# Kernel optimization log

Measured on AMD Instinct MI355X. Metric: run time of the kernel, lower is better.

## Reference

```python
import jax, jax.numpy as jnp
import numpy as np

DIM = 512

def setup_inputs() -> dict:
    key = jax.random.key(0)
    ks = jax.random.split(key, 8)
    B, T, S, D = 4, 128, 512, DIM
    scale = 1.0 / np.sqrt(D)
    return {
        "inp": jax.random.normal(ks[0], (B, T, D), jnp.float32),
        "context": jax.random.normal(ks[1], (B, S, D), jnp.float32),
        # linear_query: Linear(D, D, bias=True)
        "Wq": jax.random.normal(ks[2], (D, D), jnp.float32) * scale,
        "bq": jax.random.normal(ks[3], (D,), jnp.float32) * scale,
        # linear_context: Linear(D, D, bias=False)
        "Wc": jax.random.normal(ks[4], (D, D), jnp.float32) * scale,
        # v: Linear(D, 1, bias=False)
        "v": jax.random.normal(ks[5], (D,), jnp.float32) * scale,
        # linear_out: Linear(2D, D, bias=True)
        "Wout": jax.random.normal(ks[6], (D, 2 * D), jnp.float32) * scale,
        "bout": jax.random.normal(ks[7], (D,), jnp.float32) * scale,
    }

def reference(inp, context, Wq, bq, Wc, v, Wout, bout):
    # inp: (B,T,D) target queries; context: (B,S,D) source states
    wq = jnp.einsum('btd,ed->bte', inp, Wq) + bq          # (B,T,D)
    uh = jnp.einsum('bsd,ed->bse', context, Wc)            # (B,S,D)
    # additive (Bahdanau) score: v^T tanh(Wq q_t + Wc h_s)
    wquh = jnp.tanh(wq[:, :, None, :] + uh[:, None, :, :])  # (B,T,S,D)
    align = jnp.einsum('btsd,d->bts', wquh, v)             # (B,T,S)
    align_vectors = jax.nn.softmax(align, axis=-1)          # softmax over src_len
    c = jnp.einsum('bts,bsd->btd', align_vectors, context)  # context vector
    concat_c = jnp.concatenate([c, inp], axis=-1)           # (B,T,2D)
    attn_h = jnp.einsum('btf,ef->bte', concat_c, Wout) + bout  # (B,T,D)
    return attn_h, align_vectors
```

## Files before the change

### kernel.cpp

```cpp
#include <hip/hip_runtime.h>
#include <hip/hip_bf16.h>
#include <math.h>


typedef __attribute__((ext_vector_type(8))) short short8;
typedef __attribute__((ext_vector_type(4))) float f32x4;
typedef unsigned short ushort_t;

static __device__ __forceinline__ unsigned short f2bf(float x) {
    union { __hip_bfloat16 h; unsigned short u; } c;
    c.h = __float2bfloat16(x);
    return c.u;
}
static __device__ __forceinline__ int bf2x(float lo, float hi) {
    return (int)(((unsigned)f2bf(hi) << 16) | (unsigned)f2bf(lo));
}

template<bool BF>
static __device__ __forceinline__ void load16(const void* base, size_t elemoff,
                                              int4& r0, int4& r1) {
    if (BF) {
        const int4* p = (const int4*)((const ushort_t*)base + elemoff);
        r0 = p[0]; r1 = p[1];
    } else {
        const float4* p = (const float4*)((const float*)base + elemoff);
        float4 a = p[0], b = p[1], c = p[2], d = p[3];
        r0.x = bf2x(a.x, a.y); r0.y = bf2x(a.z, a.w);
        r0.z = bf2x(b.x, b.y); r0.w = bf2x(b.z, b.w);
        r1.x = bf2x(c.x, c.y); r1.y = bf2x(c.z, c.w);
        r1.z = bf2x(d.x, d.y); r1.w = bf2x(d.z, d.w);
    }
}

template<bool A_BF, bool W_BF, int EPI>
static __device__ __forceinline__ void gemm_body(
    ushort_t* As, ushort_t* Ws,
    const void* A, const void* W, const float* bias, const float* partial,
    void* Cv, int K, int lda, int ldw, int ldc, int bm, int bn)
{
    const int tid = threadIdx.x;
    const int wave = tid >> 6, lane = tid & 63;
    const int mh = (wave & 1) * 32, nh = (wave >> 1) * 32;
    const int quad = lane >> 4, l16 = lane & 15;
    const int srow = tid >> 2, schunk = tid & 3;

    const size_t aoff = (size_t)(bm + srow) * lda + schunk * 16;
    const size_t woff = (size_t)(bn + srow) * ldw + schunk * 16;
    int4* AsW = (int4*)&As[srow * 72 + schunk * 16];
    int4* WsW = (int4*)&Ws[srow * 72 + schunk * 16];

    f32x4 acc00 = {0.f, 0.f, 0.f, 0.f}, acc01 = acc00, acc10 = acc00, acc11 = acc00;

    int4 a0r, a1r, w0r, w1r;
    load16<A_BF>(A, aoff, a0r, a1r);
    load16<W_BF>(W, woff, w0r, w1r);

    for (int k0 = 0; k0 < K; k0 += 64) {
        AsW[0] = a0r; AsW[1] = a1r;
        WsW[0] = w0r; WsW[1] = w1r;
        __syncthreads();
        if (k0 + 64 < K) {
            load16<A_BF>(A, aoff + k0 + 64, a0r, a1r);
            load16<W_BF>(W, woff + k0 + 64, w0r, w1r);
        }
        #pragma unroll
        for (int kk = 0; kk < 64; kk += 32) {
            short8 a0 = *(const short8*)&As[(mh + l16) * 72 + kk + quad * 8];
            short8 a1 = *(const short8*)&As[(mh + 16 + l16) * 72 + kk + quad * 8];
            short8 b0 = *(const short8*)&Ws[(nh + l16) * 72 + kk + quad * 8];
            short8 b1 = *(const short8*)&Ws[(nh + 16 + l16) * 72 + kk + quad * 8];
            acc00 = __builtin_amdgcn_mfma_f32_16x16x32_bf16(a0, b0, acc00, 0, 0, 0);
            acc01 = __builtin_amdgcn_mfma_f32_16x16x32_bf16(a0, b1, acc01, 0, 0, 0);
            acc10 = __builtin_amdgcn_mfma_f32_16x16x32_bf16(a1, b0, acc10, 0, 0, 0);
            acc11 = __builtin_amdgcn_mfma_f32_16x16x32_bf16(a1, b1, acc11, 0, 0, 0);
        }
        __syncthreads();
    }

    const int col0 = bn + nh + l16;
    const int col1 = col0 + 16;
    float bias0 = bias ? bias[col0] : 0.f;
    float bias1 = bias ? bias[col1] : 0.f;

    f32x4 accs[2][2] = {{acc00, acc01}, {acc10, acc11}};
    #pragma unroll
    for (int mt = 0; mt < 2; ++mt) {
        #pragma unroll
        for (int r = 0; r < 4; ++r) {
            int row = bm + mh + mt * 16 + quad * 4 + r;
            size_t rowoff = (size_t)row * ldc;
            float v0 = accs[mt][0][r] + bias0;
            float v1 = accs[mt][1][r] + bias1;
            if (EPI == 1) { v0 = __expf(2.f * v0); v1 = __expf(2.f * v1); }
            if (EPI == 3) { v0 += partial[rowoff + col0]; v1 += partial[rowoff + col1]; }
            if (EPI == 2) {
                ushort_t* C = (ushort_t*)Cv;
                C[rowoff + col0] = f2bf(v0);
                C[rowoff + col1] = f2bf(v1);
            } else {
                float* C = (float*)Cv;
                C[rowoff + col0] = v0;
                C[rowoff + col1] = v1;
            }
        }
    }
}

__global__ __launch_bounds__(256) void fused_front(
    const float* __restrict__ inp, const float* __restrict__ ctx,
    const float* __restrict__ Wq, const float* __restrict__ bq,
    const float* __restrict__ Wc, const float* __restrict__ Wout,
    const float* __restrict__ bout,
    float* __restrict__ Ew, float* __restrict__ Eu, float* __restrict__ Y0,
    ushort_t* __restrict__ ctxT)
{
    __shared__ ushort_t As[64 * 72];
    __shared__ ushort_t Ws[64 * 72];
    __shared__ float tile[32][33];
    const int bid = blockIdx.x, tid = threadIdx.x;

    if (bid < 64) {
        gemm_body<false, false, 1>(As, Ws, inp, Wq, bq, nullptr, Ew,
                                   512, 512, 512, 512, (bid & 7) * 64, (bid >> 3) * 64);
    } else if (bid < 320) {
        int i = bid - 64;
        gemm_body<false, false, 1>(As, Ws, ctx, Wc, nullptr, nullptr, Eu,
                                   512, 512, 512, 512, (i & 31) * 64, (i >> 5) * 64);
    } else if (bid < 384) {
        int i = bid - 320;
        gemm_body<false, false, 0>(As, Ws, inp, Wout + 512, bout, nullptr, Y0,
                                   512, 512, 1024, 512, (i & 7) * 64, (i >> 3) * 64);
    } else {
        int r = bid - 384;
        int b = r >> 8;
        int tr = (r >> 4) & 15, tc = r & 15;
        const float* src = ctx + ((size_t)(b * 512 + tr * 32)) * 512 + tc * 32;
        int row8 = tid >> 5, col = tid & 31;
        #pragma unroll
        for (int p = 0; p < 4; ++p) {
            int rr = p * 8 + row8;
            tile[rr][col] = src[rr * 512 + col];
        }
        __syncthreads();
        ushort_t* dst = ctxT + ((size_t)(b * 512 + tc * 32)) * 512 + tr * 32;
        #pragma unroll
        for (int p = 0; p < 4; ++p) {
            int rr = p * 8 + row8;
            dst[rr * 512 + col] = f2bf(tile[col][rr]);
        }
    }
}

__global__ __launch_bounds__(256) void align_kernel(
    const float* __restrict__ Ew, const float* __restrict__ Eu,
    const float* __restrict__ v, float* __restrict__ out)
{
    const int lane = threadIdx.x & 63, wave = threadIdx.x >> 6;
    const int b = blockIdx.z;
    const int t0 = blockIdx.y * 8 + wave * 2;
    const int s0 = blockIdx.x * 8;

    const float* w0p = Ew + (((size_t)(b * 128 + t0)) << 9);
    const float* w1p = w0p + 512;
    const float* up  = Eu + (((size_t)(b * 512 + s0)) << 9);

    float acc0[8], acc1[8];
    #pragma unroll
    for (int j = 0; j < 8; ++j) { acc0[j] = 0.f; acc1[j] = 0.f; }
    float vsum = 0.f;

    for (int k0 = 0; k0 < 512; k0 += 64) {
        float vk = v[k0 + lane];
        vsum += vk;
        float w0 = w0p[k0 + lane];
        float w1 = w1p[k0 + lane];
        #pragma unroll
        for (int j = 0; j < 8; ++j) {
            float u = up[((size_t)j << 9) + k0 + lane];
            float d0 = fmaf(w0, u, 1.f);
            float d1 = fmaf(w1, u, 1.f);
            float r0 = __builtin_amdgcn_rcpf(d0);
            float r1 = __builtin_amdgcn_rcpf(d1);
            acc0[j] = fmaf(vk, r0, acc0[j]);
            acc1[j] = fmaf(vk, r1, acc1[j]);
        }
    }

    float V = vsum;
    #pragma unroll
    for (int off = 32; off; off >>= 1) V += __shfl_xor(V, off, 64);

    float r0 = 0.f, r1 = 0.f;
    #pragma unroll
    for (int j = 0; j < 8; ++j) {
        float a = acc0[j], c = acc1[j];
        #pragma unroll
        for (int off = 32; off; off >>= 1) {
            a += __shfl_xor(a, off, 64);
            c += __shfl_xor(c, off, 64);
        }
        if (lane == j) { r0 = fmaf(-2.f, a, V); r1 = fmaf(-2.f, c, V); }
    }
    if (lane < 8) {
        size_t o = (((size_t)(b * 128 + t0)) << 9) + s0 + lane;
        out[o] = r0;
        out[o + 512] = r1;
    }
}

__global__ __launch_bounds__(256) void softmax_512(
    float* __restrict__ data, ushort_t* __restrict__ pbf)
{
    const int row = blockIdx.x;
    float* p = data + ((size_t)row << 9);
    ushort_t* q = pbf + ((size_t)row << 9);
    const int tid = threadIdx.x;
    float x0 = p[tid];
    float x1 = p[tid + 256];

    float m = fmaxf(x0, x1);
    #pragma unroll
    for (int off = 32; off > 0; off >>= 1)
        m = fmaxf(m, __shfl_xor(m, off, 64));
    __shared__ float redm[4];
    __shared__ float reds[4];
    const int wave = tid >> 6;
    if ((tid & 63) == 0) redm[wave] = m;
    __syncthreads();
    m = fmaxf(fmaxf(redm[0], redm[1]), fmaxf(redm[2], redm[3]));

    float e0 = __expf(x0 - m);
    float e1 = __expf(x1 - m);
    float s = e0 + e1;
    #pragma unroll
    for (int off = 32; off > 0; off >>= 1)
        s += __shfl_xor(s, off, 64);
    if ((tid & 63) == 0) reds[wave] = s;
    __syncthreads();
    s = reds[0] + reds[1] + reds[2] + reds[3];
    float r = 1.0f / s;
    float p0 = e0 * r, p1 = e1 * r;
    p[tid] = p0;
    p[tid + 256] = p1;
    q[tid] = f2bf(p0);
    q[tid + 256] = f2bf(p1);
}

__global__ __launch_bounds__(256) void gemm_c(
    const ushort_t* __restrict__ P, const ushort_t* __restrict__ ctxT,
    ushort_t* __restrict__ cbf)
{
    __shared__ ushort_t As[64 * 72];
    __shared__ ushort_t Ws[64 * 72];
    const int b = blockIdx.z;
    gemm_body<true, true, 2>(As, Ws, P + (size_t)b * 65536, ctxT + (size_t)b * 262144,
                             nullptr, nullptr, cbf + (size_t)b * 65536,
                             512, 512, 512, 512, blockIdx.x * 64, blockIdx.y * 64);
}

__global__ __launch_bounds__(256) void gemm_out(
    const ushort_t* __restrict__ cbf, const float* __restrict__ Wout,
    const float* __restrict__ Y0, float* __restrict__ attn)
{
    __shared__ ushort_t As[64 * 72];
    __shared__ ushort_t Ws[64 * 72];
    gemm_body<true, false, 3>(As, Ws, cbf, Wout, nullptr, Y0, attn,
                              512, 512, 1024, 512, blockIdx.x * 64, blockIdx.y * 64);
}

extern "C" void kernel_launch(void* const* d_in, const int* in_sizes, int n_in,
                              void* d_out, int out_size, void* d_ws, size_t ws_size,
                              hipStream_t stream)
{
    const float* inp  = (const float*)d_in[0];
    const float* ctx  = (const float*)d_in[1];
    const float* Wq   = (const float*)d_in[2];
    const float* bq   = (const float*)d_in[3];
    const float* Wc   = (const float*)d_in[4];
    const float* v    = (const float*)d_in[5];
    const float* Wout = (const float*)d_in[6];
    const float* bout = (const float*)d_in[7];

    float* out   = (float*)d_out;
    float* attn  = out;
    float* align = out + 262144;

    float* ws = (float*)d_ws;
    float* Ew = ws;
    float* Eu = ws + 262144;
    float* Y0 = ws + 1310720;
    ushort_t* ub   = (ushort_t*)(ws + 1572864);
    ushort_t* ctxT = ub;
    ushort_t* P_bf = ub + 1048576;
    ushort_t* c_bf = P_bf + 262144;

    fused_front<<<dim3(1408), 256, 0, stream>>>(inp, ctx, Wq, bq, Wc, Wout, bout,
                                                Ew, Eu, Y0, ctxT);
    align_kernel<<<dim3(64, 16, 4), 256, 0, stream>>>(Ew, Eu, v, align);
    softmax_512<<<dim3(512), 256, 0, stream>>>(align, P_bf);
    gemm_c<<<dim3(2, 8, 4), 256, 0, stream>>>(P_bf, ctxT, c_bf);
    gemm_out<<<dim3(8, 8), 256, 0, stream>>>(c_bf, Wout, Y0, attn);
}
```

Before: 124.5 us.

## Reassociate context-output GEMM and fuse softmax into the attention GEMM

Precomputes G = Wout_c · context^T per batch in the front kernel, replacing the ctx transpose blocks. Attention output then becomes P · G plus Y0 in a single GEMM. Softmax is computed inside that GEMM's prologue, which writes align_vectors and converts P to bf16 on the fly. This removes the separate softmax and two-stage c/out GEMMs, cutting two launches and intermediate traffic. In exchange the front kernel does an extra 512x512x512 GEMM per batch, and the softmax row statistics are recomputed redundantly by every column-tile block.

```diff
diff --git a/kernel.cpp b/kernel.cpp
--- a/kernel.cpp
+++ b/kernel.cpp
@@ -35,7 +35,7 @@
 template<bool A_BF, bool W_BF, int EPI>
 static __device__ __forceinline__ void gemm_body(
     ushort_t* As, ushort_t* Ws,
-    const void* A, const void* W, const float* bias, const float* partial,
+    const void* A, const void* W, const float* bias,
     void* Cv, int K, int lda, int ldw, int ldc, int bm, int bn)
 {
     const int tid = threadIdx.x;
@@ -92,7 +92,6 @@
             float v0 = accs[mt][0][r] + bias0;
             float v1 = accs[mt][1][r] + bias1;
             if (EPI == 1) { v0 = __expf(2.f * v0); v1 = __expf(2.f * v1); }
-            if (EPI == 3) { v0 += partial[rowoff + col0]; v1 += partial[rowoff + col1]; }
             if (EPI == 2) {
                 ushort_t* C = (ushort_t*)Cv;
                 C[rowoff + col0] = f2bf(v0);
@@ -112,42 +111,29 @@
     const float* __restrict__ Wc, const float* __restrict__ Wout,
     const float* __restrict__ bout,
     float* __restrict__ Ew, float* __restrict__ Eu, float* __restrict__ Y0,
-    ushort_t* __restrict__ ctxT)
+    ushort_t* __restrict__ GT)
 {
     __shared__ ushort_t As[64 * 72];
     __shared__ ushort_t Ws[64 * 72];
-    __shared__ float tile[32][33];
-    const int bid = blockIdx.x, tid = threadIdx.x;
+    const int bid = blockIdx.x;
 
     if (bid < 64) {
-        gemm_body<false, false, 1>(As, Ws, inp, Wq, bq, nullptr, Ew,
+        gemm_body<false, false, 1>(As, Ws, inp, Wq, bq, Ew,
                                    512, 512, 512, 512, (bid & 7) * 64, (bid >> 3) * 64);
     } else if (bid < 320) {
         int i = bid - 64;
-        gemm_body<false, false, 1>(As, Ws, ctx, Wc, nullptr, nullptr, Eu,
+        gemm_body<false, false, 1>(As, Ws, ctx, Wc, nullptr, Eu,
                                    512, 512, 512, 512, (i & 31) * 64, (i >> 5) * 64);
-    } else if (bid < 384) {
+    } else if (bid < 576) {
         int i = bid - 320;
-        gemm_body<false, false, 0>(As, Ws, inp, Wout + 512, bout, nullptr, Y0,
+        int b = i >> 6, j = i & 63;
+        gemm_body<false, false, 2>(As, Ws, Wout, ctx + (size_t)b * 262144, nullptr,
+                                   GT + (size_t)b * 262144,
+                                   512, 1024, 512, 512, (j & 7) * 64, (j >> 3) * 64);
+    } else {
+        int i = bid - 576;
+        gemm_body<false, false, 0>(As, Ws, inp, Wout + 512, bout, Y0,
                                    512, 512, 1024, 512, (i & 7) * 64, (i >> 3) * 64);
-    } else {
-        int r = bid - 384;
-        int b = r >> 8;
-        int tr = (r >> 4) & 15, tc = r & 15;
-        const float* src = ctx + ((size_t)(b * 512 + tr * 32)) * 512 + tc * 32;
-        int row8 = tid >> 5, col = tid & 31;
-        #pragma unroll
-        for (int p = 0; p < 4; ++p) {
-            int rr = p * 8 + row8;
-            tile[rr][col] = src[rr * 512 + col];
-        }
-        __syncthreads();
-        ushort_t* dst = ctxT + ((size_t)(b * 512 + tc * 32)) * 512 + tr * 32;
-        #pragma unroll
-        for (int p = 0; p < 4; ++p) {
-            int rr = p * 8 + row8;
-            dst[rr * 512 + col] = f2bf(tile[col][rr]);
-        }
     }
 }
 
@@ -208,64 +194,105 @@
     }
 }
 
-__global__ __launch_bounds__(256) void softmax_512(
-    float* __restrict__ data, ushort_t* __restrict__ pbf)
-{
-    const int row = blockIdx.x;
-    float* p = data + ((size_t)row << 9);
-    ushort_t* q = pbf + ((size_t)row << 9);
-    const int tid = threadIdx.x;
-    float x0 = p[tid];
-    float x1 = p[tid + 256];
-
-    float m = fmaxf(x0, x1);
-    #pragma unroll
-    for (int off = 32; off > 0; off >>= 1)
-        m = fmaxf(m, __shfl_xor(m, off, 64));
-    __shared__ float redm[4];
-    __shared__ float reds[4];
-    const int wave = tid >> 6;
-    if ((tid & 63) == 0) redm[wave] = m;
-    __syncthreads();
-    m = fmaxf(fmaxf(redm[0], redm[1]), fmaxf(redm[2], redm[3]));
-
-    float e0 = __expf(x0 - m);
-    float e1 = __expf(x1 - m);
-    float s = e0 + e1;
-    #pragma unroll
-    for (int off = 32; off > 0; off >>= 1)
-        s += __shfl_xor(s, off, 64);
-    if ((tid & 63) == 0) reds[wave] = s;
-    __syncthreads();
-    s = reds[0] + reds[1] + reds[2] + reds[3];
-    float r = 1.0f / s;
-    float p0 = e0 * r, p1 = e1 * r;
-    p[tid] = p0;
-    p[tid + 256] = p1;
-    q[tid] = f2bf(p0);
-    q[tid + 256] = f2bf(p1);
-}
-
-__global__ __launch_bounds__(256) void gemm_c(
-    const ushort_t* __restrict__ P, const ushort_t* __restrict__ ctxT,
-    ushort_t* __restrict__ cbf)
+__global__ __launch_bounds__(256) void gemm_att(
+    const float* __restrict__ Sraw, const ushort_t* __restrict__ GT,
+    const float* __restrict__ Y0, float* __restrict__ attn,
+    float* __restrict__ alignv)
 {
     __shared__ ushort_t As[64 * 72];
     __shared__ ushort_t Ws[64 * 72];
+    const int tid = threadIdx.x;
     const int b = blockIdx.z;
-    gemm_body<true, true, 2>(As, Ws, P + (size_t)b * 65536, ctxT + (size_t)b * 262144,
-                             nullptr, nullptr, cbf + (size_t)b * 65536,
-                             512, 512, 512, 512, blockIdx.x * 64, blockIdx.y * 64);
-}
-
-__global__ __launch_bounds__(256) void gemm_out(
-    const ushort_t* __restrict__ cbf, const float* __restrict__ Wout,
-    const float* __restrict__ Y0, float* __restrict__ attn)
-{
-    __shared__ ushort_t As[64 * 72];
-    __shared__ ushort_t Ws[64 * 72];
-    gemm_body<true, false, 3>(As, Ws, cbf, Wout, nullptr, Y0, attn,
-                              512, 512, 1024, 512, blockIdx.x * 64, blockIdx.y * 64);
+    const int bm = blockIdx.x * 64;
+    const int bn = blockIdx.y * 64;
+    const int wave = tid >> 6, lane = tid & 63;
+    const int mh = (wave & 1) * 32, nh = (wave >> 1) * 32;
+    const int quad = lane >> 4, l16 = lane & 15;
+    const int srow = tid >> 2, schunk = tid & 3;
+
+    const float* Srow = Sraw + (((size_t)(b * 128 + bm + srow)) << 9);
+
+    const float4* qv = (const float4*)(Srow + schunk * 128);
+    float mloc = -3.4e38f;
+    #pragma unroll
+    for (int i = 0; i < 32; ++i) {
+        float4 x = qv[i];
+        mloc = fmaxf(mloc, fmaxf(fmaxf(x.x, x.y), fmaxf(x.z, x.w)));
+    }
+    mloc = fmaxf(mloc, __shfl_xor(mloc, 1, 64));
+    mloc = fmaxf(mloc, __shfl_xor(mloc, 2, 64));
+    float ssum = 0.f;
+    #pragma unroll
+    for (int i = 0; i < 32; ++i) {
+        float4 x = qv[i];
+        ssum += __expf(x.x - mloc) + __expf(x.y - mloc)
+              + __expf(x.z - mloc) + __expf(x.w - mloc);
+    }
+    ssum += __shfl_xor(ssum, 1, 64);
+    ssum += __shfl_xor(ssum, 2, 64);
+    const float rinv = __builtin_amdgcn_rcpf(ssum);
+
+    const bool wr = (blockIdx.y == 0);
+    float* arow = alignv + (((size_t)(b * 128 + bm + srow)) << 9);
+    const ushort_t* GTb = GT + (size_t)b * 262144;
+    const size_t woff = (size_t)(bn + srow) * 512 + schunk * 16;
+    int4* AsW = (int4*)&As[srow * 72 + schunk * 16];
+    int4* WsW = (int4*)&Ws[srow * 72 + schunk * 16];
+
+    f32x4 acc00 = {0.f, 0.f, 0.f, 0.f}, acc01 = acc00, acc10 = acc00, acc11 = acc00;
+
+    for (int k0 = 0; k0 < 512; k0 += 64) {
+        const float4* ap = (const float4*)(Srow + k0 + schunk * 16);
+        float4 x0 = ap[0], x1 = ap[1], x2 = ap[2], x3 = ap[3];
+        float4 p0, p1, p2, p3;
+        p0.x = __expf(x0.x - mloc) * rinv; p0.y = __expf(x0.y - mloc) * rinv;
+        p0.z = __expf(x0.z - mloc) * rinv; p0.w = __expf(x0.w - mloc) * rinv;
+        p1.x = __expf(x1.x - mloc) * rinv; p1.y = __expf(x1.y - mloc) * rinv;
+        p1.z = __expf(x1.z - mloc) * rinv; p1.w = __expf(x1.w - mloc) * rinv;
+        p2.x = __expf(x2.x - mloc) * rinv; p2.y = __expf(x2.y - mloc) * rinv;
+        p2.z = __expf(x2.z - mloc) * rinv; p2.w = __expf(x2.w - mloc) * rinv;
+        p3.x = __expf(x3.x - mloc) * rinv; p3.y = __expf(x3.y - mloc) * rinv;
+        p3.z = __expf(x3.z - mloc) * rinv; p3.w = __expf(x3.w - mloc) * rinv;
+        int4 w0r, w1r;
+        load16<true>(GTb, woff + k0, w0r, w1r);
+        if (wr) {
+            float4* d = (float4*)(arow + k0 + schunk * 16);
+            d[0] = p0; d[1] = p1; d[2] = p2; d[3] = p3;
+        }
+        int4 a0r, a1r;
+        a0r.x = bf2x(p0.x, p0.y); a0r.y = bf2x(p0.z, p0.w);
+        a0r.z = bf2x(p1.x, p1.y); a0r.w = bf2x(p1.z, p1.w);
+        a1r.x = bf2x(p2.x, p2.y); a1r.y = bf2x(p2.z, p2.w);
+        a1r.z = bf2x(p3.x, p3.y); a1r.w = bf2x(p3.z, p3.w);
+        __syncthreads();
+        AsW[0] = a0r; AsW[1] = a1r;
+        WsW[0] = w0r; WsW[1] = w1r;
+        __syncthreads();
+        #pragma unroll
+        for (int kk = 0; kk < 64; kk += 32) {
+            short8 a0 = *(const short8*)&As[(mh + l16) * 72 + kk + quad * 8];
+            short8 a1 = *(const short8*)&As[(mh + 16 + l16) * 72 + kk + quad * 8];
+            short8 b0 = *(const short8*)&Ws[(nh + l16) * 72 + kk + quad * 8];
+            short8 b1 = *(const short8*)&Ws[(nh + 16 + l16) * 72 + kk + quad * 8];
+            acc00 = __builtin_amdgcn_mfma_f32_16x16x32_bf16(a0, b0, acc00, 0, 0, 0);
+            acc01 = __builtin_amdgcn_mfma_f32_16x16x32_bf16(a0, b1, acc01, 0, 0, 0);
+            acc10 = __builtin_amdgcn_mfma_f32_16x16x32_bf16(a1, b0, acc10, 0, 0, 0);
+            acc11 = __builtin_amdgcn_mfma_f32_16x16x32_bf16(a1, b1, acc11, 0, 0, 0);
+        }
+    }
+
+    const int col0 = bn + nh + l16;
+    const int col1 = col0 + 16;
+    f32x4 accs[2][2] = {{acc00, acc01}, {acc10, acc11}};
+    #pragma unroll
+    for (int mt = 0; mt < 2; ++mt) {
+        #pragma unroll
+        for (int r = 0; r < 4; ++r) {
+            size_t rowoff = (size_t)(b * 128 + bm + mh + mt * 16 + quad * 4 + r) << 9;
+            attn[rowoff + col0] = accs[mt][0][r] + Y0[rowoff + col0];
+            attn[rowoff + col1] = accs[mt][1][r] + Y0[rowoff + col1];
+        }
+    }
 }
 
 extern "C" void kernel_launch(void* const* d_in, const int* in_sizes, int n_in,
@@ -286,18 +313,14 @@
     float* align = out + 262144;
 
     float* ws = (float*)d_ws;
-    float* Ew = ws;
-    float* Eu = ws + 262144;
-    float* Y0 = ws + 1310720;
-    ushort_t* ub   = (ushort_t*)(ws + 1572864);
-    ushort_t* ctxT = ub;
-    ushort_t* P_bf = ub + 1048576;
-    ushort_t* c_bf = P_bf + 262144;
-
-    fused_front<<<dim3(1408), 256, 0, stream>>>(inp, ctx, Wq, bq, Wc, Wout, bout,
-                                                Ew, Eu, Y0, ctxT);
-    align_kernel<<<dim3(64, 16, 4), 256, 0, stream>>>(Ew, Eu, v, align);
-    softmax_512<<<dim3(512), 256, 0, stream>>>(align, P_bf);
-    gemm_c<<<dim3(2, 8, 4), 256, 0, stream>>>(P_bf, ctxT, c_bf);
-    gemm_out<<<dim3(8, 8), 256, 0, stream>>>(c_bf, Wout, Y0, attn);
-}
+    float* Ew   = ws;
+    float* Eu   = ws + 262144;
+    float* Y0   = ws + 1310720;
+    float* Sraw = ws + 1572864;
+    ushort_t* GT = (ushort_t*)(ws + 1835008);
+
+    fused_front<<<dim3(640), 256, 0, stream>>>(inp, ctx, Wq, bq, Wc, Wout, bout,
+                                               Ew, Eu, Y0, GT);
+    align_kernel<<<dim3(64, 16, 4), 256, 0, stream>>>(Ew, Eu, v, Sraw);
+    gemm_att<<<dim3(2, 8, 4), 256, 0, stream>>>(Sraw, GT, Y0, attn, align);
+}
```

Measured after the change: 127.6 us. 2.5% more time.

## Reassociate output GEMM via Wout·ctx and fuse align, softmax and output

Applied to the files above, without the earlier changes.

Reassociates the output projection: instead of computing c = P·ctx and then c·Wout_c, it precomputes G = Wout_c·ctx^T per batch (bf16) in the front kernel, replacing the transpose blocks. A single per-row kernel then computes alignment scores, the softmax and attn = P·G^T + Y0, which removes three launches and the round trips for the score and probability buffers. The cost is extra GEMM work in the front kernel (4×512×512×512). The per-row kernel also re-reads all of Eu and G for every one of the 512 rows and has only 512 blocks, so locality and per-block work change a lot.

```diff
diff --git a/kernel.cpp b/kernel.cpp
--- a/kernel.cpp
+++ b/kernel.cpp
@@ -14,6 +14,9 @@
 }
 static __device__ __forceinline__ int bf2x(float lo, float hi) {
     return (int)(((unsigned)f2bf(hi) << 16) | (unsigned)f2bf(lo));
+}
+static __device__ __forceinline__ float bfu_as_f(unsigned u) {
+    union { unsigned u; float f; } c; c.u = u; return c.f;
 }
 
 template<bool BF>
@@ -35,7 +38,7 @@
 template<bool A_BF, bool W_BF, int EPI>
 static __device__ __forceinline__ void gemm_body(
     ushort_t* As, ushort_t* Ws,
-    const void* A, const void* W, const float* bias, const float* partial,
+    const void* A, const void* W, const float* bias,
     void* Cv, int K, int lda, int ldw, int ldc, int bm, int bn)
 {
     const int tid = threadIdx.x;
@@ -92,7 +95,6 @@
             float v0 = accs[mt][0][r] + bias0;
             float v1 = accs[mt][1][r] + bias1;
             if (EPI == 1) { v0 = __expf(2.f * v0); v1 = __expf(2.f * v1); }
-            if (EPI == 3) { v0 += partial[rowoff + col0]; v1 += partial[rowoff + col1]; }
             if (EPI == 2) {
                 ushort_t* C = (ushort_t*)Cv;
                 C[rowoff + col0] = f2bf(v0);
@@ -112,160 +114,139 @@
     const float* __restrict__ Wc, const float* __restrict__ Wout,
     const float* __restrict__ bout,
     float* __restrict__ Ew, float* __restrict__ Eu, float* __restrict__ Y0,
-    ushort_t* __restrict__ ctxT)
+    ushort_t* __restrict__ GT)
 {
     __shared__ ushort_t As[64 * 72];
     __shared__ ushort_t Ws[64 * 72];
-    __shared__ float tile[32][33];
-    const int bid = blockIdx.x, tid = threadIdx.x;
+    const int bid = blockIdx.x;
 
     if (bid < 64) {
-        gemm_body<false, false, 1>(As, Ws, inp, Wq, bq, nullptr, Ew,
+        gemm_body<false, false, 1>(As, Ws, inp, Wq, bq, Ew,
                                    512, 512, 512, 512, (bid & 7) * 64, (bid >> 3) * 64);
     } else if (bid < 320) {
         int i = bid - 64;
-        gemm_body<false, false, 1>(As, Ws, ctx, Wc, nullptr, nullptr, Eu,
+        gemm_body<false, false, 1>(As, Ws, ctx, Wc, nullptr, Eu,
                                    512, 512, 512, 512, (i & 31) * 64, (i >> 5) * 64);
-    } else if (bid < 384) {
+    } else if (bid < 576) {
         int i = bid - 320;
-        gemm_body<false, false, 0>(As, Ws, inp, Wout + 512, bout, nullptr, Y0,
+        int b = i >> 6, j = i & 63;
+        gemm_body<false, false, 2>(As, Ws, Wout, ctx + (size_t)b * 262144, nullptr,
+                                   GT + (size_t)b * 262144,
+                                   512, 1024, 512, 512, (j & 7) * 64, (j >> 3) * 64);
+    } else {
+        int i = bid - 576;
+        gemm_body<false, false, 0>(As, Ws, inp, Wout + 512, bout, Y0,
                                    512, 512, 1024, 512, (i & 7) * 64, (i >> 3) * 64);
-    } else {
-        int r = bid - 384;
-        int b = r >> 8;
-        int tr = (r >> 4) & 15, tc = r & 15;
-        const float* src = ctx + ((size_t)(b * 512 + tr * 32)) * 512 + tc * 32;
-        int row8 = tid >> 5, col = tid & 31;
-        #pragma unroll
-        for (int p = 0; p < 4; ++p) {
-            int rr = p * 8 + row8;
-            tile[rr][col] = src[rr * 512 + col];
-        }
-        __syncthreads();
-        ushort_t* dst = ctxT + ((size_t)(b * 512 + tc * 32)) * 512 + tr * 32;
-        #pragma unroll
-        for (int p = 0; p < 4; ++p) {
-            int rr = p * 8 + row8;
-            dst[rr * 512 + col] = f2bf(tile[col][rr]);
-        }
-    }
-}
-
-__global__ __launch_bounds__(256) void align_kernel(
+    }
+}
+
+__global__ __launch_bounds__(256) void fused_align(
     const float* __restrict__ Ew, const float* __restrict__ Eu,
-    const float* __restrict__ v, float* __restrict__ out)
-{
-    const int lane = threadIdx.x & 63, wave = threadIdx.x >> 6;
-    const int b = blockIdx.z;
-    const int t0 = blockIdx.y * 8 + wave * 2;
-    const int s0 = blockIdx.x * 8;
-
-    const float* w0p = Ew + (((size_t)(b * 128 + t0)) << 9);
-    const float* w1p = w0p + 512;
-    const float* up  = Eu + (((size_t)(b * 512 + s0)) << 9);
-
-    float acc0[8], acc1[8];
-    #pragma unroll
-    for (int j = 0; j < 8; ++j) { acc0[j] = 0.f; acc1[j] = 0.f; }
-    float vsum = 0.f;
-
-    for (int k0 = 0; k0 < 512; k0 += 64) {
-        float vk = v[k0 + lane];
-        vsum += vk;
-        float w0 = w0p[k0 + lane];
-        float w1 = w1p[k0 + lane];
-        #pragma unroll
-        for (int j = 0; j < 8; ++j) {
-            float u = up[((size_t)j << 9) + k0 + lane];
-            float d0 = fmaf(w0, u, 1.f);
-            float d1 = fmaf(w1, u, 1.f);
+    const float* __restrict__ v, const ushort_t* __restrict__ GT,
+    const float* __restrict__ Y0, float* __restrict__ attn,
+    float* __restrict__ alignv)
+{
+    __shared__ float sc[512];
+    __shared__ float Pf[512];
+    __shared__ float redm[4];
+    __shared__ float reds[4];
+
+    const int tid = threadIdx.x;
+    const int lane = tid & 63, w = tid >> 6;
+    const int b = blockIdx.x >> 7;
+    const int row = blockIdx.x;
+
+    const float* EwRow = Ew + ((size_t)row << 9);
+    float Ewr[8], vr[8];
+    float vloc = 0.f;
+    #pragma unroll
+    for (int c = 0; c < 8; ++c) {
+        Ewr[c] = EwRow[c * 64 + lane];
+        vr[c]  = v[c * 64 + lane];
+        vloc  += vr[c];
+    }
+    float V = vloc;
+    #pragma unroll
+    for (int off = 32; off; off >>= 1) V += __shfl_xor(V, off, 64);
+
+    const float* Eub = Eu + (((size_t)b) << 18);
+    for (int si = 0; si < 128; si += 2) {
+        int s0 = w * 128 + si;
+        const float* u0 = Eub + ((size_t)s0 << 9);
+        const float* u1 = u0 + 512;
+        float a0 = 0.f, a1 = 0.f;
+        #pragma unroll
+        for (int c = 0; c < 8; ++c) {
+            float x0 = u0[c * 64 + lane];
+            float x1 = u1[c * 64 + lane];
+            float d0 = fmaf(Ewr[c], x0, 1.f);
+            float d1 = fmaf(Ewr[c], x1, 1.f);
             float r0 = __builtin_amdgcn_rcpf(d0);
             float r1 = __builtin_amdgcn_rcpf(d1);
-            acc0[j] = fmaf(vk, r0, acc0[j]);
-            acc1[j] = fmaf(vk, r1, acc1[j]);
-        }
-    }
-
-    float V = vsum;
-    #pragma unroll
-    for (int off = 32; off; off >>= 1) V += __shfl_xor(V, off, 64);
-
-    float r0 = 0.f, r1 = 0.f;
-    #pragma unroll
-    for (int j = 0; j < 8; ++j) {
-        float a = acc0[j], c = acc1[j];
+            a0 = fmaf(vr[c], r0, a0);
+            a1 = fmaf(vr[c], r1, a1);
+        }
         #pragma unroll
         for (int off = 32; off; off >>= 1) {
-            a += __shfl_xor(a, off, 64);
-            c += __shfl_xor(c, off, 64);
-        }
-        if (lane == j) { r0 = fmaf(-2.f, a, V); r1 = fmaf(-2.f, c, V); }
-    }
-    if (lane < 8) {
-        size_t o = (((size_t)(b * 128 + t0)) << 9) + s0 + lane;
-        out[o] = r0;
-        out[o + 512] = r1;
-    }
-}
-
-__global__ __launch_bounds__(256) void softmax_512(
-    float* __restrict__ data, ushort_t* __restrict__ pbf)
-{
-    const int row = blockIdx.x;
-    float* p = data + ((size_t)row << 9);
-    ushort_t* q = pbf + ((size_t)row << 9);
-    const int tid = threadIdx.x;
-    float x0 = p[tid];
-    float x1 = p[tid + 256];
-
+            a0 += __shfl_xor(a0, off, 64);
+            a1 += __shfl_xor(a1, off, 64);
+        }
+        if (lane == 0) sc[s0]     = fmaf(-2.f, a0, V);
+        if (lane == 1) sc[s0 + 1] = fmaf(-2.f, a1, V);
+    }
+    __syncthreads();
+
+    float x0 = sc[tid];
+    float x1 = sc[tid + 256];
     float m = fmaxf(x0, x1);
     #pragma unroll
-    for (int off = 32; off > 0; off >>= 1)
-        m = fmaxf(m, __shfl_xor(m, off, 64));
-    __shared__ float redm[4];
-    __shared__ float reds[4];
-    const int wave = tid >> 6;
-    if ((tid & 63) == 0) redm[wave] = m;
+    for (int off = 32; off; off >>= 1) m = fmaxf(m, __shfl_xor(m, off, 64));
+    if (lane == 0) redm[w] = m;
     __syncthreads();
     m = fmaxf(fmaxf(redm[0], redm[1]), fmaxf(redm[2], redm[3]));
-
     float e0 = __expf(x0 - m);
     float e1 = __expf(x1 - m);
     float s = e0 + e1;
     #pragma unroll
-    for (int off = 32; off > 0; off >>= 1)
-        s += __shfl_xor(s, off, 64);
-    if ((tid & 63) == 0) reds[wave] = s;
+    for (int off = 32; off; off >>= 1) s += __shfl_xor(s, off, 64);
+    if (lane == 0) reds[w] = s;
     __syncthreads();
     s = reds[0] + reds[1] + reds[2] + reds[3];
-    float r = 1.0f / s;
-    float p0 = e0 * r, p1 = e1 * r;
-    p[tid] = p0;
-    p[tid + 256] = p1;
-    q[tid] = f2bf(p0);
-    q[tid + 256] = f2bf(p1);
-}
-
-__global__ __launch_bounds__(256) void gemm_c(
-    const ushort_t* __restrict__ P, const ushort_t* __restrict__ ctxT,
-    ushort_t* __restrict__ cbf)
-{
-    __shared__ ushort_t As[64 * 72];
-    __shared__ ushort_t Ws[64 * 72];
-    const int b = blockIdx.z;
-    gemm_body<true, true, 2>(As, Ws, P + (size_t)b * 65536, ctxT + (size_t)b * 262144,
-                             nullptr, nullptr, cbf + (size_t)b * 65536,
-                             512, 512, 512, 512, blockIdx.x * 64, blockIdx.y * 64);
-}
-
-__global__ __launch_bounds__(256) void gemm_out(
-    const ushort_t* __restrict__ cbf, const float* __restrict__ Wout,
-    const float* __restrict__ Y0, float* __restrict__ attn)
-{
-    __shared__ ushort_t As[64 * 72];
-    __shared__ ushort_t Ws[64 * 72];
-    gemm_body<true, false, 3>(As, Ws, cbf, Wout, nullptr, Y0, attn,
-                              512, 512, 1024, 512, blockIdx.x * 64, blockIdx.y * 64);
+    float rinv = 1.0f / s;
+    float p0 = e0 * rinv, p1 = e1 * rinv;
+    float* arow = alignv + ((size_t)row << 9);
+    arow[tid] = p0;
+    arow[tid + 256] = p1;
+    Pf[tid] = p0;
+    Pf[tid + 256] = p1;
+    __syncthreads();
+
+    const unsigned* GTb = (const unsigned*)(GT + (((size_t)b) << 18));
+    const float* yrow = Y0 + ((size_t)row << 9);
+    float* orow = attn + ((size_t)row << 9);
+    for (int ni = 0; ni < 128; ni += 2) {
+        int n0 = w * 128 + ni;
+        const unsigned* g0 = GTb + (n0 << 8);
+        const unsigned* g1 = g0 + 256;
+        float a0 = 0.f, a1 = 0.f;
+        #pragma unroll
+        for (int c = 0; c < 4; ++c) {
+            unsigned u0 = g0[c * 64 + lane];
+            unsigned u1 = g1[c * 64 + lane];
+            float2 pp = *(const float2*)&Pf[c * 128 + lane * 2];
+            float g0lo = bfu_as_f(u0 << 16), g0hi = bfu_as_f(u0 & 0xffff0000u);
+            float g1lo = bfu_as_f(u1 << 16), g1hi = bfu_as_f(u1 & 0xffff0000u);
+            a0 = fmaf(pp.x, g0lo, a0); a0 = fmaf(pp.y, g0hi, a0);
+            a1 = fmaf(pp.x, g1lo, a1); a1 = fmaf(pp.y, g1hi, a1);
+        }
+        #pragma unroll
+        for (int off = 32; off; off >>= 1) {
+            a0 += __shfl_xor(a0, off, 64);
+            a1 += __shfl_xor(a1, off, 64);
+        }
+        if (lane == 0) orow[n0]     = a0 + yrow[n0];
+        if (lane == 1) orow[n0 + 1] = a1 + yrow[n0 + 1];
+    }
 }
 
 extern "C" void kernel_launch(void* const* d_in, const int* in_sizes, int n_in,
@@ -281,23 +262,17 @@
     const float* Wout = (const float*)d_in[6];
     const float* bout = (const float*)d_in[7];
 
-    float* out   = (float*)d_out;
-    float* attn  = out;
-    float* align = out + 262144;
+    float* out    = (float*)d_out;
+    float* attn   = out;
+    float* alignv = out + 262144;
 
     float* ws = (float*)d_ws;
-    float* Ew = ws;
-    float* Eu = ws + 262144;
-    float* Y0 = ws + 1310720;
-    ushort_t* ub   = (ushort_t*)(ws + 1572864);
-    ushort_t* ctxT = ub;
-    ushort_t* P_bf = ub + 1048576;
-    ushort_t* c_bf = P_bf + 262144;
-
-    fused_front<<<dim3(1408), 256, 0, stream>>>(inp, ctx, Wq, bq, Wc, Wout, bout,
-                                                Ew, Eu, Y0, ctxT);
-    align_kernel<<<dim3(64, 16, 4), 256, 0, stream>>>(Ew, Eu, v, align);
-    softmax_512<<<dim3(512), 256, 0, stream>>>(align, P_bf);
-    gemm_c<<<dim3(2, 8, 4), 256, 0, stream>>>(P_bf, ctxT, c_bf);
-    gemm_out<<<dim3(8, 8), 256, 0, stream>>>(c_bf, Wout, Y0, attn);
-}
+    float* Ew   = ws;
+    float* Eu   = ws + 262144;
+    float* Y0   = ws + 1310720;
+    ushort_t* GT = (ushort_t*)(ws + 1572864);
+
+    fused_front<<<dim3(640), 256, 0, stream>>>(inp, ctx, Wq, bq, Wc, Wout, bout,
+                                               Ew, Eu, Y0, GT);
+    fused_align<<<dim3(512), 256, 0, stream>>>(Ew, Eu, v, GT, Y0, attn, alignv);
+}
```

Result: slower. 180.6 us (+45.0%).

## Fold Wout into context before softmax, fuse attn GEMMs, widen align tile

Applied to the files above, without the earlier changes.

The front kernel now computes G = Wout_c·context per batch as a bf16 transposed operand, replacing the plain context transpose. After softmax, a single GEMM P·G plus Y0 produces attn directly, which removes the separate c GEMM and out GEMM and one launch. The align kernel now processes four query rows per wave instead of two, reusing each context row load across more queries, and softmax reads from a workspace buffer instead of working in place. The cost is extra front work (a 512x512x512 GEMM per batch) and more registers per align thread.

```diff
diff --git a/kernel.cpp b/kernel.cpp
--- a/kernel.cpp
+++ b/kernel.cpp
@@ -112,12 +112,11 @@
     const float* __restrict__ Wc, const float* __restrict__ Wout,
     const float* __restrict__ bout,
     float* __restrict__ Ew, float* __restrict__ Eu, float* __restrict__ Y0,
-    ushort_t* __restrict__ ctxT)
+    ushort_t* __restrict__ GT)
 {
     __shared__ ushort_t As[64 * 72];
     __shared__ ushort_t Ws[64 * 72];
-    __shared__ float tile[32][33];
-    const int bid = blockIdx.x, tid = threadIdx.x;
+    const int bid = blockIdx.x;
 
     if (bid < 64) {
         gemm_body<false, false, 1>(As, Ws, inp, Wq, bq, nullptr, Ew,
@@ -126,28 +125,16 @@
         int i = bid - 64;
         gemm_body<false, false, 1>(As, Ws, ctx, Wc, nullptr, nullptr, Eu,
                                    512, 512, 512, 512, (i & 31) * 64, (i >> 5) * 64);
-    } else if (bid < 384) {
+    } else if (bid < 576) {
         int i = bid - 320;
+        int b = i >> 6, j = i & 63;
+        gemm_body<false, false, 2>(As, Ws, Wout, ctx + (size_t)b * 262144, nullptr,
+                                   nullptr, GT + (size_t)b * 262144,
+                                   512, 1024, 512, 512, (j & 7) * 64, (j >> 3) * 64);
+    } else {
+        int i = bid - 576;
         gemm_body<false, false, 0>(As, Ws, inp, Wout + 512, bout, nullptr, Y0,
                                    512, 512, 1024, 512, (i & 7) * 64, (i >> 3) * 64);
-    } else {
-        int r = bid - 384;
-        int b = r >> 8;
-        int tr = (r >> 4) & 15, tc = r & 15;
-        const float* src = ctx + ((size_t)(b * 512 + tr * 32)) * 512 + tc * 32;
-        int row8 = tid >> 5, col = tid & 31;
-        #pragma unroll
-        for (int p = 0; p < 4; ++p) {
-            int rr = p * 8 + row8;
-            tile[rr][col] = src[rr * 512 + col];
-        }
-        __syncthreads();
-        ushort_t* dst = ctxT + ((size_t)(b * 512 + tc * 32)) * 512 + tr * 32;
-        #pragma unroll
-        for (int p = 0; p < 4; ++p) {
-            int rr = p * 8 + row8;
-            dst[rr * 512 + col] = f2bf(tile[col][rr]);
-        }
     }
 }
 
@@ -157,32 +144,41 @@
 {
     const int lane = threadIdx.x & 63, wave = threadIdx.x >> 6;
     const int b = blockIdx.z;
-    const int t0 = blockIdx.y * 8 + wave * 2;
+    const int t0 = blockIdx.y * 16 + wave * 4;
     const int s0 = blockIdx.x * 8;
 
-    const float* w0p = Ew + (((size_t)(b * 128 + t0)) << 9);
-    const float* w1p = w0p + 512;
-    const float* up  = Eu + (((size_t)(b * 512 + s0)) << 9);
-
-    float acc0[8], acc1[8];
-    #pragma unroll
-    for (int j = 0; j < 8; ++j) { acc0[j] = 0.f; acc1[j] = 0.f; }
+    const float* wp = Ew + (((size_t)(b * 128 + t0)) << 9);
+    const float* up = Eu + (((size_t)(b * 512 + s0)) << 9);
+
+    float acc[4][8];
+    #pragma unroll
+    for (int i = 0; i < 4; ++i)
+        #pragma unroll
+        for (int j = 0; j < 8; ++j) acc[i][j] = 0.f;
     float vsum = 0.f;
 
     for (int k0 = 0; k0 < 512; k0 += 64) {
         float vk = v[k0 + lane];
         vsum += vk;
-        float w0 = w0p[k0 + lane];
-        float w1 = w1p[k0 + lane];
+        float w0 = wp[k0 + lane];
+        float w1 = wp[512 + k0 + lane];
+        float w2 = wp[1024 + k0 + lane];
+        float w3 = wp[1536 + k0 + lane];
         #pragma unroll
         for (int j = 0; j < 8; ++j) {
             float u = up[((size_t)j << 9) + k0 + lane];
             float d0 = fmaf(w0, u, 1.f);
             float d1 = fmaf(w1, u, 1.f);
+            float d2 = fmaf(w2, u, 1.f);
+            float d3 = fmaf(w3, u, 1.f);
             float r0 = __builtin_amdgcn_rcpf(d0);
             float r1 = __builtin_amdgcn_rcpf(d1);
-            acc0[j] = fmaf(vk, r0, acc0[j]);
-            acc1[j] = fmaf(vk, r1, acc1[j]);
+            float r2 = __builtin_amdgcn_rcpf(d2);
+            float r3 = __builtin_amdgcn_rcpf(d3);
+            acc[0][j] = fmaf(vk, r0, acc[0][j]);
+            acc[1][j] = fmaf(vk, r1, acc[1][j]);
+            acc[2][j] = fmaf(vk, r2, acc[2][j]);
+            acc[3][j] = fmaf(vk, r3, acc[3][j]);
         }
     }
 
@@ -190,29 +186,40 @@
     #pragma unroll
     for (int off = 32; off; off >>= 1) V += __shfl_xor(V, off, 64);
 
-    float r0 = 0.f, r1 = 0.f;
+    float r0 = 0.f, r1 = 0.f, r2 = 0.f, r3 = 0.f;
     #pragma unroll
     for (int j = 0; j < 8; ++j) {
-        float a = acc0[j], c = acc1[j];
+        float a0 = acc[0][j], a1 = acc[1][j], a2 = acc[2][j], a3 = acc[3][j];
         #pragma unroll
         for (int off = 32; off; off >>= 1) {
-            a += __shfl_xor(a, off, 64);
-            c += __shfl_xor(c, off, 64);
-        }
-        if (lane == j) { r0 = fmaf(-2.f, a, V); r1 = fmaf(-2.f, c, V); }
+            a0 += __shfl_xor(a0, off, 64);
+            a1 += __shfl_xor(a1, off, 64);
+            a2 += __shfl_xor(a2, off, 64);
+            a3 += __shfl_xor(a3, off, 64);
+        }
+        if (lane == j) {
+            r0 = fmaf(-2.f, a0, V);
+            r1 = fmaf(-2.f, a1, V);
+            r2 = fmaf(-2.f, a2, V);
+            r3 = fmaf(-2.f, a3, V);
+        }
     }
     if (lane < 8) {
         size_t o = (((size_t)(b * 128 + t0)) << 9) + s0 + lane;
         out[o] = r0;
         out[o + 512] = r1;
+        out[o + 1024] = r2;
+        out[o + 1536] = r3;
     }
 }
 
 __global__ __launch_bounds__(256) void softmax_512(
-    float* __restrict__ data, ushort_t* __restrict__ pbf)
+    const float* __restrict__ Sraw, float* __restrict__ alignv,
+    ushort_t* __restrict__ pbf)
 {
     const int row = blockIdx.x;
-    float* p = data + ((size_t)row << 9);
+    const float* p = Sraw + ((size_t)row << 9);
+    float* a = alignv + ((size_t)row << 9);
     ushort_t* q = pbf + ((size_t)row << 9);
     const int tid = threadIdx.x;
     float x0 = p[tid];
@@ -240,32 +247,24 @@
     s = reds[0] + reds[1] + reds[2] + reds[3];
     float r = 1.0f / s;
     float p0 = e0 * r, p1 = e1 * r;
-    p[tid] = p0;
-    p[tid + 256] = p1;
+    a[tid] = p0;
+    a[tid + 256] = p1;
     q[tid] = f2bf(p0);
     q[tid + 256] = f2bf(p1);
 }
 
-__global__ __launch_bounds__(256) void gemm_c(
-    const ushort_t* __restrict__ P, const ushort_t* __restrict__ ctxT,
-    ushort_t* __restrict__ cbf)
+__global__ __launch_bounds__(256) void gemm_att(
+    const ushort_t* __restrict__ P, const ushort_t* __restrict__ GT,
+    const float* __restrict__ Y0, float* __restrict__ attn)
 {
     __shared__ ushort_t As[64 * 72];
     __shared__ ushort_t Ws[64 * 72];
     const int b = blockIdx.z;
-    gemm_body<true, true, 2>(As, Ws, P + (size_t)b * 65536, ctxT + (size_t)b * 262144,
-                             nullptr, nullptr, cbf + (size_t)b * 65536,
+    gemm_body<true, true, 3>(As, Ws,
+                             P + (size_t)b * 65536, GT + (size_t)b * 262144,
+                             nullptr, Y0 + (size_t)b * 65536,
+                             attn + (size_t)b * 65536,
                              512, 512, 512, 512, blockIdx.x * 64, blockIdx.y * 64);
-}
-
-__global__ __launch_bounds__(256) void gemm_out(
-    const ushort_t* __restrict__ cbf, const float* __restrict__ Wout,
-    const float* __restrict__ Y0, float* __restrict__ attn)
-{
-    __shared__ ushort_t As[64 * 72];
-    __shared__ ushort_t Ws[64 * 72];
-    gemm_body<true, false, 3>(As, Ws, cbf, Wout, nullptr, Y0, attn,
-                              512, 512, 1024, 512, blockIdx.x * 64, blockIdx.y * 64);
 }
 
 extern "C" void kernel_launch(void* const* d_in, const int* in_sizes, int n_in,
@@ -281,23 +280,21 @@
     const float* Wout = (const float*)d_in[6];
     const float* bout = (const float*)d_in[7];
 
-    float* out   = (float*)d_out;
-    float* attn  = out;
-    float* align = out + 262144;
+    float* out    = (float*)d_out;
+    float* attn   = out;
+    float* alignv = out + 262144;
 
     float* ws = (float*)d_ws;
-    float* Ew = ws;
-    float* Eu = ws + 262144;
-    float* Y0 = ws + 1310720;
-    ushort_t* ub   = (ushort_t*)(ws + 1572864);
-    ushort_t* ctxT = ub;
-    ushort_t* P_bf = ub + 1048576;
-    ushort_t* c_bf = P_bf + 262144;
-
-    fused_front<<<dim3(1408), 256, 0, stream>>>(inp, ctx, Wq, bq, Wc, Wout, bout,
-                                                Ew, Eu, Y0, ctxT);
-    align_kernel<<<dim3(64, 16, 4), 256, 0, stream>>>(Ew, Eu, v, align);
-    softmax_512<<<dim3(512), 256, 0, stream>>>(align, P_bf);
-    gemm_c<<<dim3(2, 8, 4), 256, 0, stream>>>(P_bf, ctxT, c_bf);
-    gemm_out<<<dim3(8, 8), 256, 0, stream>>>(c_bf, Wout, Y0, attn);
-}
+    float* Ew   = ws;
+    float* Eu   = ws + 262144;
+    float* Y0   = ws + 1310720;
+    float* Sraw = ws + 1572864;
+    ushort_t* GT   = (ushort_t*)(ws + 1835008);
+    ushort_t* P_bf = (ushort_t*)(ws + 2359296);
+
+    fused_front<<<dim3(640), 256, 0, stream>>>(inp, ctx, Wq, bq, Wc, Wout, bout,
+                                               Ew, Eu, Y0, GT);
+    align_kernel<<<dim3(64, 8, 4), 256, 0, stream>>>(Ew, Eu, v, Sraw);
+    softmax_512<<<dim3(512), 256, 0, stream>>>(Sraw, alignv, P_bf);
+    gemm_att<<<dim3(2, 8, 4), 256, 0, stream>>>(P_bf, GT, Y0, attn);
+}
```

Result: faster. 121.4 us (-2.5%).
